# Performance work log

Measured on AMD Instinct MI355X. Metric: run time of the kernel, lower is better.

The kernel has to match this reference:

```python
import jax, jax.numpy as jnp
import numpy as np

B, L, DW, DP = 128, 512, 256, 64
NF = 512          # num_filters == types == nr (forced by U.view / maxpool in source)
D = DW + 2 * DP   # 384
DWIN = 3 * D      # windowed feature width


def setup_inputs() -> dict:
    key = jax.random.key(0)
    ks = jax.random.split(key, 10)
    return {
        "x": jax.random.normal(ks[0], (B, L, DW), jnp.float32),
        "e1": jax.random.normal(ks[1], (B, DW), jnp.float32),
        "e2": jax.random.normal(ks[2], (B, DW), jnp.float32),
        "posVec": jax.random.normal(ks[3], (B, L, 2 * DP), jnp.float32),
        "We1": jax.random.normal(ks[4], (DW, DW), jnp.float32),
        "We2": jax.random.normal(ks[5], (DW, DW), jnp.float32),
        "U": jax.random.normal(ks[6], (NF, NF), jnp.float32),
        "conv_w": jax.random.normal(ks[7], (NF, DWIN), jnp.float32) * 0.02,
        "conv_b": jnp.zeros((NF,), jnp.float32),
        "rel_w": jax.random.normal(ks[8], (NF, NF), jnp.float32) * 0.02,  # y_embedding.weight (nr, num_filters)
    }


def reference(x, e1, e2, posVec, We1, We2, U, conv_w, conv_b, rel_w):
    # ---- input attention ----
    x_concat = jnp.concatenate([x, posVec], axis=-1)            # (B, L, D)
    px = jnp.pad(x_concat, ((0, 0), (1, 1), (0, 0)))            # pad seq by k=1
    w_concat = jnp.concatenate(
        [px[:, 0:L], px[:, 1:L + 1], px[:, 2:L + 2]], axis=-1)  # (B, L, 3D)
    A1 = jnp.einsum('bld,de,be->bl', x, We1, e1)                # (B, L)
    A2 = jnp.einsum('bld,de,be->bl', x, We2, e2)
    alpha = 0.5 * (jax.nn.softmax(A1, axis=1) + jax.nn.softmax(A2, axis=1))
    R = w_concat * alpha[:, :, None]                            # (B, L, 3D)
    # ---- convolution (kernel spans full window -> per-position linear) ----
    conv = jnp.tanh(jnp.einsum('bld,fd->bfl', R, conv_w) + conv_b[None, :, None])  # (B, F, L)
    # ---- attentive pooling ----
    G = jnp.einsum('bfl,ft,rt->blr', conv, U, rel_w)            # (B, L, nr)
    AP = jax.nn.softmax(G, axis=1)                              # softmax over seq positions
    wo = jnp.einsum('bfl,blr->bfr', conv, AP)                   # (B, F, nr)
    wo = jnp.max(wo, axis=2)                                    # MaxPool2d((1, types)) -> (B, F)
    wo = jax.nn.relu(wo)
    return wo, rel_w
```

## Files before the change

### kernel.cpp

```cpp
#include <hip/hip_runtime.h>
#include <hip/hip_bf16.h>

#define BB 128
#define LL 512
#define DW 256
#define DP 64
#define NF 512
#define DD 384
#define DWIN 1152
#define RR 512
#define LP 514

typedef __attribute__((ext_vector_type(8))) short short8;
typedef __attribute__((ext_vector_type(4))) short short4v;
typedef __attribute__((ext_vector_type(2))) short short2v;
typedef __attribute__((ext_vector_type(8))) _Float16 half8;
typedef __attribute__((ext_vector_type(4))) float f32x4;
typedef __attribute__((ext_vector_type(2))) float f32x2;

typedef __attribute__((address_space(1))) const void* gas_t;
typedef __attribute__((address_space(3))) void* las_t;

__device__ __forceinline__ void stage16(const void* g, void* l) {
    __builtin_amdgcn_global_load_lds((gas_t)g, (las_t)l, 16, 0, 0);
}

__device__ inline short f2h(float v) {
    _Float16 h = (_Float16)v;
    return *reinterpret_cast<short*>(&h);
}
__device__ inline int xcd_swz(int bid, int nwg) {
    return (bid & 7) * (nwg >> 3) + (bid >> 3);
}

__global__ void k_ve(const float* __restrict__ We1, const float* __restrict__ We2,
                     const float* __restrict__ e1, const float* __restrict__ e2,
                     float* __restrict__ v1, float* __restrict__ v2) {
    int b = blockIdx.x;
    int d = threadIdx.x;
    __shared__ float s1[DW], s2[DW];
    s1[d] = e1[b * DW + d];
    s2[d] = e2[b * DW + d];
    __syncthreads();
    float a1 = 0.f, a2 = 0.f;
    for (int e = 0; e < DW; ++e) {
        a1 += We1[d * DW + e] * s1[e];
        a2 += We2[d * DW + e] * s2[e];
    }
    v1[b * DW + d] = a1;
    v2[b * DW + d] = a2;
}

__global__ __launch_bounds__(256) void k_pack_logits(
    const float* __restrict__ x, const float* __restrict__ pv,
    const float* __restrict__ v1, const float* __restrict__ v2,
    short* __restrict__ pxp, float* __restrict__ A1, float* __restrict__ A2) {
    int gr = blockIdx.x * 4 + (threadIdx.x >> 6);
    int lane = threadIdx.x & 63;
    int b = gr / LP;
    int rr = gr - b * LP;
    short* dst = pxp + (size_t)gr * DD;
    if (rr == 0 || rr == LP - 1) {
        *(short4v*)(dst + lane * 4) = (short4v){0, 0, 0, 0};
        *(short2v*)(dst + 256 + lane * 2) = (short2v){0, 0};
        return;
    }
    int l = rr - 1;
    f32x4 xv = *(const f32x4*)(x + ((size_t)b * LL + l) * DW + lane * 4);
    f32x2 pvv = *(const f32x2*)(pv + ((size_t)b * LL + l) * (2 * DP) + lane * 2);
    f32x4 w1 = *(const f32x4*)(v1 + b * DW + lane * 4);
    f32x4 w2 = *(const f32x4*)(v2 + b * DW + lane * 4);
    float p1 = xv[0] * w1[0] + xv[1] * w1[1] + xv[2] * w1[2] + xv[3] * w1[3];
    float p2 = xv[0] * w2[0] + xv[1] * w2[1] + xv[2] * w2[2] + xv[3] * w2[3];
    for (int off = 32; off; off >>= 1) {
        p1 += __shfl_down(p1, off);
        p2 += __shfl_down(p2, off);
    }
    short4v ox;
#pragma unroll
    for (int j = 0; j < 4; ++j) ox[j] = f2h(xv[j]);
    *(short4v*)(dst + lane * 4) = ox;
    short2v op;
    op[0] = f2h(pvv[0]);
    op[1] = f2h(pvv[1]);
    *(short2v*)(dst + 256 + lane * 2) = op;
    if (lane == 0) { A1[b * LL + l] = p1; A2[b * LL + l] = p2; }
}

__global__ void k_alpha(const float* __restrict__ A1, const float* __restrict__ A2,
                        float* __restrict__ alpha) {
    int b = blockIdx.x;
    int l = threadIdx.x;
    __shared__ float s[LL];
    float a1 = A1[b * LL + l], a2 = A2[b * LL + l];

    s[l] = a1; __syncthreads();
    for (int st = 256; st; st >>= 1) { if (l < st) s[l] = fmaxf(s[l], s[l + st]); __syncthreads(); }
    float m1 = s[0]; __syncthreads();
    float e1x = expf(a1 - m1);
    s[l] = e1x; __syncthreads();
    for (int st = 256; st; st >>= 1) { if (l < st) s[l] += s[l + st]; __syncthreads(); }
    float d1 = s[0]; __syncthreads();

    s[l] = a2; __syncthreads();
    for (int st = 256; st; st >>= 1) { if (l < st) s[l] = fmaxf(s[l], s[l + st]); __syncthreads(); }
    float m2 = s[0]; __syncthreads();
    float e2x = expf(a2 - m2);
    s[l] = e2x; __syncthreads();
    for (int st = 256; st; st >>= 1) { if (l < st) s[l] += s[l + st]; __syncthreads(); }
    float d2 = s[0];

    alpha[b * LL + l] = 0.5f * (e1x / d1 + e2x / d2);
}

__global__ __launch_bounds__(256) void k_pack_w(const float* __restrict__ cw,
                                                short* __restrict__ cwb) {
    int idx = blockIdx.x * 256 + threadIdx.x;
    const float* src = cw + (size_t)idx * 8;
    f32x4 u0 = *(const f32x4*)(src);
    f32x4 u1 = *(const f32x4*)(src + 4);
    short8 v;
#pragma unroll
    for (int jj = 0; jj < 4; ++jj) { v[jj] = f2h(u0[jj]); v[jj + 4] = f2h(u1[jj]); }
    *(short8*)(cwb + (size_t)idx * 8) = v;
}

__global__ void k_w2t(const float* __restrict__ U, const float* __restrict__ relw,
                      short* __restrict__ Qf) {
    __shared__ float As[16][65], Bs[16][65];
    int r0 = blockIdx.y * 64, f0 = blockIdx.x * 64;
    int tid = threadIdx.x, ty = tid >> 4, tx = tid & 15;
    float acc[4][4] = {};
    for (int k0 = 0; k0 < NF; k0 += 16) {
        for (int i = 0; i < 4; ++i) {
            int lin = tid + 256 * i;
            int kk = lin & 15, mm = lin >> 4;
            As[kk][mm] = relw[(r0 + mm) * NF + k0 + kk];
            Bs[kk][mm] = U[(f0 + mm) * NF + k0 + kk];
        }
        __syncthreads();
        for (int kk = 0; kk < 16; ++kk) {
            float av[4], bv[4];
            for (int i = 0; i < 4; ++i) av[i] = As[kk][ty * 4 + i];
            for (int j = 0; j < 4; ++j) bv[j] = Bs[kk][tx * 4 + j];
            for (int i = 0; i < 4; ++i)
                for (int j = 0; j < 4; ++j) acc[i][j] += av[i] * bv[j];
        }
        __syncthreads();
    }
    for (int i = 0; i < 4; ++i)
        for (int j = 0; j < 4; ++j)
            Qf[(size_t)(r0 + ty * 4 + i) * NF + f0 + tx * 4 + j] = f2h(acc[i][j]);
}

__global__ __launch_bounds__(256) void k_conv_mfma(
    const short* __restrict__ pxp, const short* __restrict__ cwb,
    const float* __restrict__ conv_b, const float* __restrict__ alpha,
    short* __restrict__ conv_lf, short* __restrict__ conv_fl) {
    int wg = xcd_swz(blockIdx.x, 2048);
    int b = wg >> 4;
    int l0 = ((wg >> 2) & 3) * 128;
    int f0 = (wg & 3) * 128;
    int tid = threadIdx.x;
    int lane = tid & 63, w = tid >> 6;
    int wm = w >> 1, wn = w & 1;
    int lr = lane & 15, lg = lane >> 4;

    __shared__ __align__(16) char smem[34816];
    short (*As)[32] = (short(*)[32])smem;
    short (*Bs)[32] = (short(*)[32])(smem + 8192);
    short (*T)[136] = (short(*)[136])smem;

    f32x4 acc[4][4];
    for (int i = 0; i < 4; ++i)
        for (int j = 0; j < 4; ++j) acc[i][j] = (f32x4){0.f, 0.f, 0.f, 0.f};

    int rowA = lane >> 2;
    int sw = (lane & 3) ^ ((rowA >> 1) & 3);
    const short* gA = pxp + ((size_t)b * LP + l0 + w * 32 + rowA) * DD + sw * 8;
    const short* gB = cwb + (size_t)(f0 + w * 32 + rowA) * DWIN + sw * 8;
    short* lA = &As[w * 32][0];
    short* lB = &Bs[w * 32][0];
    int rsw = (lg ^ ((lr >> 1) & 3)) * 8;
    int rA = wm * 64, rB = wn * 64;

    for (int kb = 0; kb < 36; ++kb) {
        int k0 = kb * 32;
        stage16(gA + k0, lA);
        stage16(gA + 16 * DD + k0, lA + 16 * 32);
        stage16(gB + k0, lB);
        stage16(gB + (size_t)16 * DWIN + k0, lB + 16 * 32);
        __syncthreads();
        half8 af[4], bf[4];
#pragma unroll
        for (int mi = 0; mi < 4; ++mi)
            af[mi] = *(const half8*)(&As[rA + mi * 16 + lr][rsw]);
#pragma unroll
        for (int ni = 0; ni < 4; ++ni)
            bf[ni] = *(const half8*)(&Bs[rB + ni * 16 + lr][rsw]);
#pragma unroll
        for (int mi = 0; mi < 4; ++mi)
#pragma unroll
            for (int ni = 0; ni < 4; ++ni)
                acc[mi][ni] = __builtin_amdgcn_mfma_f32_16x16x32_f16(
                    af[mi], bf[ni], acc[mi][ni], 0, 0, 0);
        __syncthreads();
    }

    int lbase = l0 + wm * 64, fbase = f0 + wn * 64;
#pragma unroll
    for (int mi = 0; mi < 4; ++mi) {
        f32x4 av = *(const f32x4*)(alpha + (size_t)b * LL + lbase + mi * 16 + lg * 4);
        int lrow = lbase + mi * 16 + lg * 4;
#pragma unroll
        for (int ni = 0; ni < 4; ++ni) {
            int f = fbase + ni * 16 + lr;
            float bias = conv_b[f];
            short4v o;
#pragma unroll
            for (int r = 0; r < 4; ++r) {
                float val = tanhf(av[r] * acc[mi][ni][r] + bias);
                short sv = f2h(val);
                o[r] = sv;
                conv_lf[((size_t)b * LL + lrow + r) * NF + f] = sv;
            }
            *(short4v*)(&T[wn * 64 + ni * 16 + lr][wm * 64 + mi * 16 + lg * 4]) = o;
        }
    }
    __syncthreads();
#pragma unroll
    for (int i = 0; i < 8; ++i) {
        int lin = tid + 256 * i;
        int frow = lin >> 4;
        int q = lin & 15;
        short8 v = *(const short8*)(&T[frow][q * 8]);
        *(short8*)(conv_fl + ((size_t)b * NF + f0 + frow) * LL + l0 + q * 8) = v;
    }
}

__global__ __launch_bounds__(512) void k_g_mfma(
    const short* __restrict__ Qf,
    const short* __restrict__ convlf, _Float16* __restrict__ Gp) {
    const float LOG2E = 1.4426950408889634f;
    int wg = xcd_swz(blockIdx.x, 512);
    int b = wg >> 2;
    int r0 = (wg & 3) * 128;
    int tid = threadIdx.x, lane = tid & 63, w = tid >> 6;
    int wm = w >> 2, wn = w & 3;
    int lr = lane & 15, lg = lane >> 4;

    __shared__ __align__(16) char smem[81920];
    short* Ab = (short*)smem;
    short* Bb = (short*)(smem + 16384);
    float (*rowred)[4] = (float(*)[4])smem;

    f32x4 acc[4][8];
#pragma unroll
    for (int i = 0; i < 4; ++i)
#pragma unroll
        for (int j = 0; j < 8; ++j) acc[i][j] = (f32x4){0.f, 0.f, 0.f, 0.f};

    int trow = tid >> 3;
    int sw = (tid & 7) ^ (trow & 7);
    const short* gA = Qf + (size_t)(r0 + trow) * NF + sw * 8;
    const short* gB = convlf + (size_t)b * LL * NF + (size_t)trow * NF + sw * 8;
    short* lAd = Ab + w * 512;
    short* lBd = Bb + w * 512;
    int p7 = lr & 7;

    for (int kb = 0; kb < 8; ++kb) {
        int k0 = kb * 64;
#pragma unroll
        for (int c = 0; c < 2; ++c)
            stage16(gA + (size_t)(64 * c) * NF + k0, lAd + c * 4096);
#pragma unroll
        for (int c = 0; c < 8; ++c)
            stage16(gB + (size_t)(64 * c) * NF + k0, lBd + c * 4096);
        __syncthreads();
#pragma unroll
        for (int kk = 0; kk < 2; ++kk) {
            int cs = (kk << 2) + lg;
            half8 af[4], bf[8];
#pragma unroll
            for (int mi = 0; mi < 4; ++mi)
                af[mi] = *(const half8*)(Ab + (wm * 64 + mi * 16 + lr) * 64 + ((cs ^ p7) * 8));
#pragma unroll
            for (int ni = 0; ni < 8; ++ni)
                bf[ni] = *(const half8*)(Bb + (wn * 128 + ni * 16 + lr) * 64 + ((cs ^ p7) * 8));
#pragma unroll
            for (int mi = 0; mi < 4; ++mi)
#pragma unroll
                for (int ni = 0; ni < 8; ++ni)
                    acc[mi][ni] = __builtin_amdgcn_mfma_f32_16x16x32_f16(
                        af[mi], bf[ni], acc[mi][ni], 0, 0, 0);
        }
        __syncthreads();
    }

    float mrow[4][4];
#pragma unroll
    for (int mi = 0; mi < 4; ++mi)
#pragma unroll
        for (int rr = 0; rr < 4; ++rr) {
            float m = acc[mi][0][rr];
#pragma unroll
            for (int ni = 1; ni < 8; ++ni) m = fmaxf(m, acc[mi][ni][rr]);
            m = fmaxf(m, __shfl_xor(m, 1));
            m = fmaxf(m, __shfl_xor(m, 2));
            m = fmaxf(m, __shfl_xor(m, 4));
            m = fmaxf(m, __shfl_xor(m, 8));
            mrow[mi][rr] = m;
        }
    if (lr == 0) {
#pragma unroll
        for (int mi = 0; mi < 4; ++mi)
#pragma unroll
            for (int rr = 0; rr < 4; ++rr)
                rowred[wm * 64 + mi * 16 + lg * 4 + rr][wn] = mrow[mi][rr];
    }
    __syncthreads();
#pragma unroll
    for (int mi = 0; mi < 4; ++mi)
#pragma unroll
        for (int rr = 0; rr < 4; ++rr) {
            f32x4 rv = *(const f32x4*)rowred[wm * 64 + mi * 16 + lg * 4 + rr];
            mrow[mi][rr] = fmaxf(fmaxf(rv[0], rv[1]), fmaxf(rv[2], rv[3]));
        }
    __syncthreads();
    float srow[4][4];
#pragma unroll
    for (int mi = 0; mi < 4; ++mi)
#pragma unroll
        for (int rr = 0; rr < 4; ++rr) {
            float s = 0.f;
            float m = mrow[mi][rr];
#pragma unroll
            for (int ni = 0; ni < 8; ++ni) {
                float pp = exp2f((acc[mi][ni][rr] - m) * LOG2E);
                acc[mi][ni][rr] = pp;
                s += pp;
            }
            s += __shfl_xor(s, 1);
            s += __shfl_xor(s, 2);
            s += __shfl_xor(s, 4);
            s += __shfl_xor(s, 8);
            srow[mi][rr] = s;
        }
    if (lr == 0) {
#pragma unroll
        for (int mi = 0; mi < 4; ++mi)
#pragma unroll
            for (int rr = 0; rr < 4; ++rr)
                rowred[wm * 64 + mi * 16 + lg * 4 + rr][wn] = srow[mi][rr];
    }
    __syncthreads();
#pragma unroll
    for (int mi = 0; mi < 4; ++mi)
#pragma unroll
        for (int rr = 0; rr < 4; ++rr) {
            f32x4 rv = *(const f32x4*)rowred[wm * 64 + mi * 16 + lg * 4 + rr];
            srow[mi][rr] = 1.f / (rv[0] + rv[1] + rv[2] + rv[3]);
        }

#pragma unroll
    for (int mi = 0; mi < 4; ++mi)
#pragma unroll
        for (int ni = 0; ni < 8; ++ni)
#pragma unroll
            for (int rr = 0; rr < 4; ++rr) {
                int r = r0 + wm * 64 + mi * 16 + lg * 4 + rr;
                int l = wn * 128 + ni * 16 + lr;
                Gp[((size_t)b * RR + r) * LL + l] = (_Float16)(acc[mi][ni][rr] * srow[mi][rr]);
            }
}

__global__ __launch_bounds__(256) void k_wo_mfma(
    const short* __restrict__ convfl, const short* __restrict__ P,
    float* __restrict__ out) {
    int wg = xcd_swz(blockIdx.x, 2048);
    int b = wg >> 4;
    int f0 = ((wg >> 2) & 3) * 128;
    int r0 = (wg & 3) * 128;
    int tid = threadIdx.x, lane = tid & 63, w = tid >> 6;
    int wm = w >> 1, wn = w & 1;
    int lr = lane & 15, lg = lane >> 4;

    __shared__ __align__(16) short As[128][64];
    __shared__ __align__(16) short Bs[128][64];

    f32x4 acc[4][4];
    for (int i = 0; i < 4; ++i)
        for (int j = 0; j < 4; ++j) acc[i][j] = (f32x4){0.f, 0.f, 0.f, 0.f};

    int rowA = lane >> 3;
    int sw = (lane & 7) ^ rowA;
    const short* gA = convfl + (size_t)b * NF * LL + (size_t)(f0 + w * 32 + rowA) * LL + sw * 8;
    const short* gB = P + (size_t)b * RR * LL + (size_t)(r0 + w * 32 + rowA) * LL + sw * 8;
    short* lA = &As[w * 32][0];
    short* lB = &Bs[w * 32][0];
    int rA = wm * 64, rB = wn * 64;
    int p7 = lr & 7;

    for (int kb = 0; kb < 8; ++kb) {
        int k0 = kb * 64;
#pragma unroll
        for (int c = 0; c < 4; ++c) {
            stage16(gA + (size_t)(8 * c) * LL + k0, lA + c * 8 * 64);
            stage16(gB + (size_t)(8 * c) * LL + k0, lB + c * 8 * 64);
        }
        __syncthreads();
#pragma unroll
        for (int kk = 0; kk < 2; ++kk) {
            half8 af[4], bf[4];
            int cs = ((kk << 2) + lg);
#pragma unroll
            for (int mi = 0; mi < 4; ++mi)
                af[mi] = *(const half8*)(&As[rA + mi * 16 + lr][(cs ^ p7) * 8]);
#pragma unroll
            for (int ni = 0; ni < 4; ++ni)
                bf[ni] = *(const half8*)(&Bs[rB + ni * 16 + lr][(cs ^ p7) * 8]);
#pragma unroll
            for (int mi = 0; mi < 4; ++mi)
#pragma unroll
                for (int ni = 0; ni < 4; ++ni)
                    acc[mi][ni] = __builtin_amdgcn_mfma_f32_16x16x32_f16(
                        af[mi], bf[ni], acc[mi][ni], 0, 0, 0);
        }
        __syncthreads();
    }

    int fbase = f0 + wm * 64;
#pragma unroll
    for (int mi = 0; mi < 4; ++mi)
#pragma unroll
        for (int rr = 0; rr < 4; ++rr) {
            float m = acc[mi][0][rr];
#pragma unroll
            for (int ni = 1; ni < 4; ++ni) m = fmaxf(m, acc[mi][ni][rr]);
            m = fmaxf(m, __shfl_xor(m, 1));
            m = fmaxf(m, __shfl_xor(m, 2));
            m = fmaxf(m, __shfl_xor(m, 4));
            m = fmaxf(m, __shfl_xor(m, 8));
            if (lr == 0 && m > 0.f) {
                int f = fbase + mi * 16 + lg * 4 + rr;
                atomicMax((int*)&out[(size_t)b * NF + f], __float_as_int(m));
            }
        }
}

extern "C" void kernel_launch(void* const* d_in, const int* in_sizes, int n_in,
                              void* d_out, int out_size, void* d_ws, size_t ws_size,
                              hipStream_t stream) {
    const float* x      = (const float*)d_in[0];
    const float* e1     = (const float*)d_in[1];
    const float* e2     = (const float*)d_in[2];
    const float* posVec = (const float*)d_in[3];
    const float* We1    = (const float*)d_in[4];
    const float* We2    = (const float*)d_in[5];
    const float* U      = (const float*)d_in[6];
    const float* conv_w = (const float*)d_in[7];
    const float* conv_b = (const float*)d_in[8];
    const float* rel_w  = (const float*)d_in[9];
    float* out = (float*)d_out;

    char* p = (char*)d_ws;
    short* convlf = (short*)p;  p += (size_t)BB * LL * NF * 2;
    short* convfl = (short*)p;  p += (size_t)BB * NF * LL * 2;
    _Float16* Gp  = (_Float16*)p;  p += (size_t)BB * RR * LL * 2;
    short* pxp    = (short*)p;  p += (size_t)BB * LP * DD * 2;
    short* cwb    = (short*)p;  p += (size_t)NF * DWIN * 2;
    short* QfW    = (short*)p;  p += (size_t)RR * NF * 2;
    float* v1     = (float*)p;  p += (size_t)BB * DW * 4;
    float* v2     = (float*)p;  p += (size_t)BB * DW * 4;
    float* A1     = (float*)p;  p += (size_t)BB * LL * 4;
    float* A2     = (float*)p;  p += (size_t)BB * LL * 4;
    float* alpha  = (float*)p;  p += (size_t)BB * LL * 4;

    k_ve<<<BB, DW, 0, stream>>>(We1, We2, e1, e2, v1, v2);
    k_pack_logits<<<(BB * LP) / 4, 256, 0, stream>>>(x, posVec, v1, v2, pxp, A1, A2);
    k_alpha<<<BB, LL, 0, stream>>>(A1, A2, alpha);
    k_pack_w<<<(NF * DWIN / 8) / 256, 256, 0, stream>>>(conv_w, cwb);
    k_w2t<<<dim3(NF / 64, RR / 64), 256, 0, stream>>>(U, rel_w, QfW);
    k_conv_mfma<<<2048, 256, 0, stream>>>(pxp, cwb, conv_b, alpha, convlf, convfl);
    k_g_mfma<<<512, 512, 0, stream>>>(QfW, convlf, Gp);
    hipMemsetAsync(d_out, 0, (size_t)BB * NF * sizeof(float), stream);
    k_wo_mfma<<<2048, 256, 0, stream>>>(convfl, (const short*)Gp, out);
    hipMemcpyAsync(out + BB * NF, rel_w, (size_t)NF * RR * sizeof(float),
                   hipMemcpyDeviceToDevice, stream);
}
```

Before: 328.1 us.

## Double-buffer LDS staging in conv and wo MFMA kernels to overlap loads

Converts the single-buffered global-to-LDS staging loops of the conv and attentive-pooling output GEMM kernels into a two-stage ping-pong pipeline. The next K tile is prefetched with global_load_lds while the current tile feeds the MFMAs, using explicit vmcnt waits and raw s_barrier plus sched_barrier fences in place of __syncthreads. The aim is to hide global-load latency behind compute. In exchange, LDS use per block doubles (to 64 KB in the wo kernel), which can lower occupancy, and correctness now depends on the manual waitcnt counts.

```diff
diff --git a/kernel.cpp b/kernel.cpp
--- a/kernel.cpp
+++ b/kernel.cpp
@@ -167,8 +167,6 @@
     int lr = lane & 15, lg = lane >> 4;
 
     __shared__ __align__(16) char smem[34816];
-    short (*As)[32] = (short(*)[32])smem;
-    short (*Bs)[32] = (short(*)[32])(smem + 8192);
     short (*T)[136] = (short(*)[136])smem;
 
     f32x4 acc[4][4];
@@ -179,32 +177,50 @@
     int sw = (lane & 3) ^ ((rowA >> 1) & 3);
     const short* gA = pxp + ((size_t)b * LP + l0 + w * 32 + rowA) * DD + sw * 8;
     const short* gB = cwb + (size_t)(f0 + w * 32 + rowA) * DWIN + sw * 8;
-    short* lA = &As[w * 32][0];
-    short* lB = &Bs[w * 32][0];
     int rsw = (lg ^ ((lr >> 1) & 3)) * 8;
     int rA = wm * 64, rB = wn * 64;
 
-    for (int kb = 0; kb < 36; ++kb) {
-        int k0 = kb * 32;
-        stage16(gA + k0, lA);
-        stage16(gA + 16 * DD + k0, lA + 16 * 32);
-        stage16(gB + k0, lB);
-        stage16(gB + (size_t)16 * DWIN + k0, lB + 16 * 32);
-        __syncthreads();
+    {
+        char* nbuf = smem;
+        stage16(gA, nbuf + w * 2048);
+        stage16(gA + 16 * DD, nbuf + w * 2048 + 1024);
+        stage16(gB, nbuf + 8192 + w * 2048);
+        stage16(gB + (size_t)16 * DWIN, nbuf + 8192 + w * 2048 + 1024);
+    }
+
+    for (int t = 0; t < 36; ++t) {
+        char* cbuf = smem + (t & 1) * 16384;
+        if (t + 1 < 36) {
+            char* nbuf = smem + ((t + 1) & 1) * 16384;
+            int k0 = (t + 1) * 32;
+            stage16(gA + k0, nbuf + w * 2048);
+            stage16(gA + 16 * DD + k0, nbuf + w * 2048 + 1024);
+            stage16(gB + k0, nbuf + 8192 + w * 2048);
+            stage16(gB + (size_t)16 * DWIN + k0, nbuf + 8192 + w * 2048 + 1024);
+            asm volatile("s_waitcnt vmcnt(4)" ::: "memory");
+        } else {
+            asm volatile("s_waitcnt vmcnt(0)" ::: "memory");
+        }
+        __builtin_amdgcn_s_barrier();
+        __builtin_amdgcn_sched_barrier(0);
+        const short (*Ac)[32] = (const short(*)[32])cbuf;
+        const short (*Bc)[32] = (const short(*)[32])(cbuf + 8192);
         half8 af[4], bf[4];
 #pragma unroll
         for (int mi = 0; mi < 4; ++mi)
-            af[mi] = *(const half8*)(&As[rA + mi * 16 + lr][rsw]);
+            af[mi] = *(const half8*)(&Ac[rA + mi * 16 + lr][rsw]);
 #pragma unroll
         for (int ni = 0; ni < 4; ++ni)
-            bf[ni] = *(const half8*)(&Bs[rB + ni * 16 + lr][rsw]);
+            bf[ni] = *(const half8*)(&Bc[rB + ni * 16 + lr][rsw]);
 #pragma unroll
         for (int mi = 0; mi < 4; ++mi)
 #pragma unroll
             for (int ni = 0; ni < 4; ++ni)
                 acc[mi][ni] = __builtin_amdgcn_mfma_f32_16x16x32_f16(
                     af[mi], bf[ni], acc[mi][ni], 0, 0, 0);
-        __syncthreads();
+        __builtin_amdgcn_sched_barrier(0);
+        __builtin_amdgcn_s_barrier();
+        __builtin_amdgcn_sched_barrier(0);
     }
 
     int lbase = l0 + wm * 64, fbase = f0 + wn * 64;
@@ -385,8 +401,7 @@
     int wm = w >> 1, wn = w & 1;
     int lr = lane & 15, lg = lane >> 4;
 
-    __shared__ __align__(16) short As[128][64];
-    __shared__ __align__(16) short Bs[128][64];
+    __shared__ __align__(16) char smem[65536];
 
     f32x4 acc[4][4];
     for (int i = 0; i < 4; ++i)
@@ -396,29 +411,46 @@
     int sw = (lane & 7) ^ rowA;
     const short* gA = convfl + (size_t)b * NF * LL + (size_t)(f0 + w * 32 + rowA) * LL + sw * 8;
     const short* gB = P + (size_t)b * RR * LL + (size_t)(r0 + w * 32 + rowA) * LL + sw * 8;
-    short* lA = &As[w * 32][0];
-    short* lB = &Bs[w * 32][0];
     int rA = wm * 64, rB = wn * 64;
     int p7 = lr & 7;
 
-    for (int kb = 0; kb < 8; ++kb) {
-        int k0 = kb * 64;
+    {
+        char* nbuf = smem;
 #pragma unroll
         for (int c = 0; c < 4; ++c) {
-            stage16(gA + (size_t)(8 * c) * LL + k0, lA + c * 8 * 64);
-            stage16(gB + (size_t)(8 * c) * LL + k0, lB + c * 8 * 64);
-        }
-        __syncthreads();
+            stage16(gA + (size_t)(8 * c) * LL, nbuf + w * 4096 + c * 1024);
+            stage16(gB + (size_t)(8 * c) * LL, nbuf + 16384 + w * 4096 + c * 1024);
+        }
+    }
+
+    for (int t = 0; t < 8; ++t) {
+        char* cbuf = smem + (t & 1) * 32768;
+        if (t + 1 < 8) {
+            char* nbuf = smem + ((t + 1) & 1) * 32768;
+            int k0 = (t + 1) * 64;
+#pragma unroll
+            for (int c = 0; c < 4; ++c) {
+                stage16(gA + (size_t)(8 * c) * LL + k0, nbuf + w * 4096 + c * 1024);
+                stage16(gB + (size_t)(8 * c) * LL + k0, nbuf + 16384 + w * 4096 + c * 1024);
+            }
+            asm volatile("s_waitcnt vmcnt(8)" ::: "memory");
+        } else {
+            asm volatile("s_waitcnt vmcnt(0)" ::: "memory");
+        }
+        __builtin_amdgcn_s_barrier();
+        __builtin_amdgcn_sched_barrier(0);
+        const short (*Ac)[64] = (const short(*)[64])cbuf;
+        const short (*Bc)[64] = (const short(*)[64])(cbuf + 16384);
 #pragma unroll
         for (int kk = 0; kk < 2; ++kk) {
             half8 af[4], bf[4];
             int cs = ((kk << 2) + lg);
 #pragma unroll
             for (int mi = 0; mi < 4; ++mi)
-                af[mi] = *(const half8*)(&As[rA + mi * 16 + lr][(cs ^ p7) * 8]);
+                af[mi] = *(const half8*)(&Ac[rA + mi * 16 + lr][(cs ^ p7) * 8]);
 #pragma unroll
             for (int ni = 0; ni < 4; ++ni)
-                bf[ni] = *(const half8*)(&Bs[rB + ni * 16 + lr][(cs ^ p7) * 8]);
+                bf[ni] = *(const half8*)(&Bc[rB + ni * 16 + lr][(cs ^ p7) * 8]);
 #pragma unroll
             for (int mi = 0; mi < 4; ++mi)
 #pragma unroll
@@ -426,7 +458,9 @@
                     acc[mi][ni] = __builtin_amdgcn_mfma_f32_16x16x32_f16(
                         af[mi], bf[ni], acc[mi][ni], 0, 0, 0);
         }
-        __syncthreads();
+        __builtin_amdgcn_sched_barrier(0);
+        __builtin_amdgcn_s_barrier();
+        __builtin_amdgcn_sched_barrier(0);
     }
 
     int fbase = f0 + wm * 64;
```

New measurement: 326.7 us. About the same (-0.4%).
